# Kernel tuning notes

Measured on AMD Instinct MI355X. Metric: run time of the kernel, lower is better.

The kernel has to match this reference:

```python
import jax, jax.numpy as jnp
import numpy as np

N_NODES = 100000
N_EDGES = 1600000
D = 64


def setup_inputs() -> dict:
    key = jax.random.key(0)
    k0, k1, k2, k3 = jax.random.split(key, 4)
    scale = 1.0 / np.sqrt(D)
    return {
        "x": jax.random.normal(k0, (N_NODES, D), dtype=jnp.float32),
        "W1": jax.random.normal(k1, (D, D), dtype=jnp.float32) * scale,
        "W2": jax.random.normal(k2, (D, D), dtype=jnp.float32) * scale,
        "b2": jnp.zeros((D,), dtype=jnp.float32),
        "edge_index": jax.random.randint(k3, (2, N_EDGES), 0, N_NODES, dtype=jnp.int32),
    }


def reference(x, W1, W2, b2, edge_index):
    # KapoorConv forward in eval mode (Dropout(p=0.5) is identity at inference).
    n = x.shape[0]
    # GCNConv adds self-loops, then symmetric normalization D^-1/2 A D^-1/2.
    loops = jnp.arange(n, dtype=edge_index.dtype)
    src = jnp.concatenate([edge_index[0], loops])  # message source j
    dst = jnp.concatenate([edge_index[1], loops])  # aggregation target i
    deg = jnp.zeros((n,), x.dtype).at[dst].add(jnp.float32(1.0))
    dinv = jax.lax.rsqrt(deg)  # deg >= 1 thanks to self-loops
    norm = (dinv[src] * dinv[dst])[:, None]  # [E+N, 1]

    def gcn(h, W, b):
        h = h @ W                                   # dense transform first
        msg = h[src] * norm                         # gather + normalize
        out = jax.ops.segment_sum(msg, dst, num_segments=n)  # scatter-add
        return out if b is None else out + b

    h = jax.nn.relu(gcn(x, W1, None))  # layer1: bias=False
    return gcn(h, W2, b2)              # layer2: bias=True
```

## Files before the change

### kernel.cpp

```cpp
#include <hip/hip_runtime.h>

#define D 64
#define CHUNK 8192
#define BKT_SHIFT 8
#define BKT_NODES 256
#define MAXB 512
#define CAP 8192
#define GROWS 64
#define SSTR 68

typedef unsigned int u32;

__device__ __forceinline__ u32 bfr(float v) {
    u32 x = __float_as_uint(v);
    return (x + 0x7fffu + ((x >> 16) & 1u)) >> 16;
}
__device__ __forceinline__ u32 pack2(float lo, float hi) { return bfr(lo) | (bfr(hi) << 16); }
__device__ __forceinline__ float blo(u32 w) { return __uint_as_float(w << 16); }
__device__ __forceinline__ float bhi(u32 w) { return __uint_as_float(w & 0xffff0000u); }


__global__ void init_cursor(int* __restrict__ cursor, int B) {
    int i = blockIdx.x * blockDim.x + threadIdx.x;
    if (i < B) cursor[i] = i * CAP;
}


__global__ void partition(const int* __restrict__ src, const int* __restrict__ dst,
                          int* __restrict__ cursor, int* __restrict__ packed,
                          int nE, int B) {
    __shared__ int hist[MAXB];
    __shared__ int delta[MAXB];
    __shared__ int s[MAXB];
    __shared__ int sorted[CHUNK];
    __shared__ unsigned short sortedb[CHUNK];
    int t = threadIdx.x;
    int i0 = blockIdx.x * CHUNK;
    int cn = min(CHUNK, nE - i0);

    hist[t] = 0;
    __syncthreads();
    for (int i = t; i < cn; i += 512) atomicAdd(&hist[dst[i0 + i] >> BKT_SHIFT], 1);
    __syncthreads();

    int v = hist[t];
    s[t] = v;
    __syncthreads();
    for (int off = 1; off < MAXB; off <<= 1) {
        int u = (t >= off) ? s[t - off] : 0;
        __syncthreads();
        s[t] += u;
        __syncthreads();
    }
    {
        int excl = s[t] - v;
        int rb = 0;
        if (t < B && v > 0) rb = atomicAdd(&cursor[t], v);
        delta[t] = rb - excl;
        hist[t] = excl;
    }
    __syncthreads();

    for (int i = t; i < cn; i += 512) {
        int d = dst[i0 + i];
        int b = d >> BKT_SHIFT;
        int pp = atomicAdd(&hist[b], 1);
        sorted[pp]  = ((d & (BKT_NODES - 1)) << 17) | src[i0 + i];
        sortedb[pp] = (unsigned short)b;
    }
    __syncthreads();

    for (int i = t; i < cn; i += 512) {
        packed[delta[sortedb[i]] + i] = sorted[i];
    }
}


__global__ void bucket_csr(const int* __restrict__ packed, const int* __restrict__ cursor,
                           int* __restrict__ row_ptr, float* __restrict__ dinv,
                           int* __restrict__ adj, const float* __restrict__ x,
                           u32* __restrict__ xp, int n, int B) {
    __shared__ int s[BKT_NODES];
    __shared__ int cur[BKT_NODES];
    __shared__ float dv[BKT_NODES];
    __shared__ int base_s;
    int t = threadIdx.x;
    int b = blockIdx.x;
    int rlo = b * CAP;
    int mycnt = min(cursor[b] - rlo, CAP);

    int partial = 0;
    for (int i = t; i < b; i += BKT_NODES) partial += cursor[i] - i * CAP;
    s[t] = partial;
    __syncthreads();
    for (int off = BKT_NODES / 2; off > 0; off >>= 1) {
        if (t < off) s[t] += s[t + off];
        __syncthreads();
    }
    if (t == 0) base_s = s[0];
    __syncthreads();
    int base = base_s;
    if (b == B - 1 && t == 0) row_ptr[n] = base + mycnt;

    s[t] = 0;
    __syncthreads();
    for (int i = t; i < mycnt; i += BKT_NODES) atomicAdd(&s[packed[rlo + i] >> 17], 1);
    __syncthreads();

    int v = s[t];
    __syncthreads();
    for (int off = 1; off < BKT_NODES; off <<= 1) {
        int u = (t >= off) ? s[t - off] : 0;
        __syncthreads();
        s[t] += u;
        __syncthreads();
    }
    int gbeg = base + s[t] - v;
    int node = (b << BKT_SHIFT) + t;
    float di = rsqrtf(1.0f + (float)v);
    if (node < n) {
        row_ptr[node] = gbeg;
        dinv[node] = di;
    }
    dv[t] = di;
    cur[t] = gbeg;
    __syncthreads();

    for (int i = t; i < mycnt; i += BKT_NODES) {
        int w = packed[rlo + i];
        int pos = atomicAdd(&cur[w >> 17], 1);
        adj[pos] = w & 0x1FFFF;
    }

    int nbase = b << BKT_SHIFT;
    for (int i = t; i < BKT_NODES * 8; i += BKT_NODES) {
        int row = i >> 3, fb = i & 7;
        int nd = nbase + row;
        if (nd < n) {
            float d2 = dv[row];
            const float4* xr = (const float4*)(x + (size_t)nd * D + 8 * fb);
            float4 v0 = xr[0], v1 = xr[1];
            uint4 w;
            w.x = pack2(d2 * v0.x, d2 * v0.y);
            w.y = pack2(d2 * v0.z, d2 * v0.w);
            w.z = pack2(d2 * v1.x, d2 * v1.y);
            w.w = pack2(d2 * v1.z, d2 * v1.w);
            ((uint4*)(xp + (size_t)nd * (D / 2)))[fb] = w;
        }
    }
}

template <int MODE>
__launch_bounds__(256, 4)
__global__ void fused(const u32* __restrict__ hp, const int* __restrict__ row_ptr,
                      const int* __restrict__ adj,
                      const float* __restrict__ W, const float* __restrict__ bias,
                      const float* __restrict__ dinv,
                      float* __restrict__ outf, u32* __restrict__ outb, int n) {
    __shared__ float Wl[D * D];
    __shared__ float Sl[GROWS * SSTR];
    const int t = threadIdx.x;

    for (int i = t; i < D * D / 4; i += 256)
        ((float4*)Wl)[i] = ((const float4*)W)[i];

    const int R0 = blockIdx.x * GROWS;

    const int lane = t & 63;
    const int o = lane >> 3;
    const int f = lane & 7;
    const int wv = t >> 6;

#pragma unroll
    for (int r = 0; r < 2; ++r) {
        int row = wv * 16 + r * 8 + o;
        int nq = R0 + row;
        bool valid = nq < n;
        int nqc = valid ? nq : 0;
        int rb = row_ptr[nqc];
        int re = row_ptr[nqc + 1];
        int len = valid ? (re - rb) : 0;

        uint4 sw = ((const uint4*)(hp + (size_t)nqc * (D / 2)))[f];
        float acc[8];
        acc[0] = blo(sw.x); acc[1] = bhi(sw.x);
        acc[2] = blo(sw.y); acc[3] = bhi(sw.y);
        acc[4] = blo(sw.z); acc[5] = bhi(sw.z);
        acc[6] = blo(sw.w); acc[7] = bhi(sw.w);

        int lm = len;
        lm = max(lm, __shfl_xor(lm, 8, 64));
        lm = max(lm, __shfl_xor(lm, 16, 64));
        lm = max(lm, __shfl_xor(lm, 32, 64));

        for (int base = 0; base < lm; base += 8) {
            int rem = len - base;
            int idx_l = 0;
            if (f < rem) idx_l = adj[rb + base + f];
            int ss[8]; uint4 vv[8];
#pragma unroll
            for (int u = 0; u < 8; ++u) {
                ss[u] = __shfl(idx_l, (o << 3) | u, 64);
            }
#pragma unroll
            for (int u = 0; u < 8; ++u) {
                vv[u] = ((const uint4*)(hp + (size_t)ss[u] * (D / 2)))[f];
            }
#pragma unroll
            for (int u = 0; u < 8; ++u) {
                float m = (u < rem) ? 1.0f : 0.0f;
                acc[0] = fmaf(m, blo(vv[u].x), acc[0]);
                acc[1] = fmaf(m, bhi(vv[u].x), acc[1]);
                acc[2] = fmaf(m, blo(vv[u].y), acc[2]);
                acc[3] = fmaf(m, bhi(vv[u].y), acc[3]);
                acc[4] = fmaf(m, blo(vv[u].z), acc[4]);
                acc[5] = fmaf(m, bhi(vv[u].z), acc[5]);
                acc[6] = fmaf(m, blo(vv[u].w), acc[6]);
                acc[7] = fmaf(m, bhi(vv[u].w), acc[7]);
            }
        }
        *(float4*)&Sl[row * SSTR + 8 * f]     = make_float4(acc[0], acc[1], acc[2], acc[3]);
        *(float4*)&Sl[row * SSTR + 8 * f + 4] = make_float4(acc[4], acc[5], acc[6], acc[7]);
    }
    __syncthreads();

    const int cg = t & 15;
    const int rg = t >> 4;

    float4 acc0 = make_float4(0.f, 0.f, 0.f, 0.f);
    float4 acc1 = make_float4(0.f, 0.f, 0.f, 0.f);
    float4 acc2 = make_float4(0.f, 0.f, 0.f, 0.f);
    float4 acc3 = make_float4(0.f, 0.f, 0.f, 0.f);

#pragma unroll 4
    for (int k = 0; k < D; k += 4) {
        float4 a0 = *(const float4*)&Sl[(4 * rg + 0) * SSTR + k];
        float4 a1 = *(const float4*)&Sl[(4 * rg + 1) * SSTR + k];
        float4 a2 = *(const float4*)&Sl[(4 * rg + 2) * SSTR + k];
        float4 a3 = *(const float4*)&Sl[(4 * rg + 3) * SSTR + k];
        float4 w0 = *(const float4*)&Wl[(k + 0) * D + 4 * cg];
        float4 w1 = *(const float4*)&Wl[(k + 1) * D + 4 * cg];
        float4 w2 = *(const float4*)&Wl[(k + 2) * D + 4 * cg];
        float4 w3 = *(const float4*)&Wl[(k + 3) * D + 4 * cg];
#define MAC(ACC, A)                                                        \
        ACC.x = fmaf(A.x, w0.x, fmaf(A.y, w1.x, fmaf(A.z, w2.x, fmaf(A.w, w3.x, ACC.x)))); \
        ACC.y = fmaf(A.x, w0.y, fmaf(A.y, w1.y, fmaf(A.z, w2.y, fmaf(A.w, w3.y, ACC.y)))); \
        ACC.z = fmaf(A.x, w0.z, fmaf(A.y, w1.z, fmaf(A.z, w2.z, fmaf(A.w, w3.z, ACC.z)))); \
        ACC.w = fmaf(A.x, w0.w, fmaf(A.y, w1.w, fmaf(A.z, w2.w, fmaf(A.w, w3.w, ACC.w))))
        MAC(acc0, a0);
        MAC(acc1, a1);
        MAC(acc2, a2);
        MAC(acc3, a3);
#undef MAC
    }

    const float4 bv = (MODE == 1) ? ((const float4*)bias)[cg]
                                  : make_float4(0.f, 0.f, 0.f, 0.f);
    float4 accs[4] = {acc0, acc1, acc2, acc3};
#pragma unroll
    for (int r = 0; r < 4; ++r) {
        int row = R0 + 4 * rg + r;
        if (row >= n) break;
        float dn = dinv[row];
        float4 y = accs[r];
        if (MODE == 0) {
            float o0 = dn * fmaxf(dn * y.x, 0.f);
            float o1 = dn * fmaxf(dn * y.y, 0.f);
            float o2 = dn * fmaxf(dn * y.z, 0.f);
            float o3 = dn * fmaxf(dn * y.w, 0.f);
            uint2 w2o;
            w2o.x = pack2(o0, o1);
            w2o.y = pack2(o2, o3);
            ((uint2*)(outb + (size_t)row * (D / 2)))[cg] = w2o;
        } else {
            float4 oo;
            oo.x = fmaf(dn, y.x, bv.x);
            oo.y = fmaf(dn, y.y, bv.y);
            oo.z = fmaf(dn, y.z, bv.z);
            oo.w = fmaf(dn, y.w, bv.w);
            ((float4*)(outf + (size_t)row * D))[cg] = oo;
        }
    }
}


extern "C" void kernel_launch(void* const* d_in, const int* in_sizes, int n_in,
                              void* d_out, int out_size, void* d_ws, size_t ws_size,
                              hipStream_t stream) {
    const float* x  = (const float*)d_in[0];
    const float* W1 = (const float*)d_in[1];
    const float* W2 = (const float*)d_in[2];
    const float* b2 = (const float*)d_in[3];
    const int*   ei = (const int*)d_in[4];

    int n  = in_sizes[0] / D;
    int nE = in_sizes[4] / 2;
    const int* src = ei;
    const int* dst = ei + nE;

    int B = (n + BKT_NODES - 1) >> BKT_SHIFT;

    auto align = [](size_t v) { return (v + 255) & ~(size_t)255; };
    char* ws = (char*)d_ws;
    size_t off = 0;
    int* row_ptr = (int*)(ws + off);   off += align((size_t)(n + 1) * 4);
    float* dinv  = (float*)(ws + off); off += align((size_t)n * 4);
    int* cursor  = (int*)(ws + off);   off += align((size_t)MAXB * 4);
    int* adj     = (int*)(ws + off);   off += align((size_t)nE * 4);
    int* packed  = (int*)(ws + off);   off += align((size_t)(B + 1) * CAP * 4);
    u32* F0      = (u32*)(ws + off);   off += align((size_t)n * (D / 2) * 4);
    u32* F1      = (u32*)(ws + off);
    float* out = (float*)d_out;

    int nchunks = (nE + CHUNK - 1) / CHUNK;

    init_cursor<<<2, 256, 0, stream>>>(cursor, B);
    partition<<<nchunks, 512, 0, stream>>>(src, dst, cursor, packed, nE, B);
    bucket_csr<<<B, BKT_NODES, 0, stream>>>(packed, cursor, row_ptr, dinv, adj, x, F0, n, B);

    int gblocks = (n + GROWS - 1) / GROWS;

    fused<0><<<gblocks, 256, 0, stream>>>(F0, row_ptr, adj, W1, nullptr, dinv, nullptr, F1, n);

    fused<1><<<gblocks, 256, 0, stream>>>(F1, row_ptr, adj, W2, b2, dinv, out, nullptr, n);
}
```

Before: 205.7 us.

## Replace bucketed LDS partition CSR build with global-atomic counting sort

Replaces the two-pass shared-memory bucket partition and per-bucket CSR build with a plain counting sort: global atomic degree count, a hierarchical scan over runs of 16 nodes, then a scatter using global atomic cursors. The x prescale-to-bf16 step is folded into the scatter kernel. This removes the large packed intermediate buffer and the LDS sorting, but adds more kernel launches, a single-block scan, and heavily contended global atomics with random-order writes into adj. Within-row edge order becomes nondeterministic, which can change floating-point summation order.

Result: slower. 344.0 us (+67.3%).

```diff
diff --git a/kernel.cpp b/kernel.cpp
--- a/kernel.cpp
+++ b/kernel.cpp
@@ -1,13 +1,9 @@
 #include <hip/hip_runtime.h>
 
 #define D 64
-#define CHUNK 8192
-#define BKT_SHIFT 8
-#define BKT_NODES 256
-#define MAXB 512
-#define CAP 8192
 #define GROWS 64
 #define SSTR 68
+#define RUN 16
 
 typedef unsigned int u32;
 
@@ -20,133 +16,94 @@
 __device__ __forceinline__ float bhi(u32 w) { return __uint_as_float(w & 0xffff0000u); }
 
 
-__global__ void init_cursor(int* __restrict__ cursor, int B) {
+__global__ void zero_k(int* __restrict__ p, int n) {
     int i = blockIdx.x * blockDim.x + threadIdx.x;
-    if (i < B) cursor[i] = i * CAP;
-}
-
-
-__global__ void partition(const int* __restrict__ src, const int* __restrict__ dst,
-                          int* __restrict__ cursor, int* __restrict__ packed,
-                          int nE, int B) {
-    __shared__ int hist[MAXB];
-    __shared__ int delta[MAXB];
-    __shared__ int s[MAXB];
-    __shared__ int sorted[CHUNK];
-    __shared__ unsigned short sortedb[CHUNK];
+    if (i < n) p[i] = 0;
+}
+
+__global__ void count_deg(const int* __restrict__ dst, int* __restrict__ deg, int nE) {
+    int i = blockIdx.x * blockDim.x + threadIdx.x;
+    if (i < nE) atomicAdd(&deg[dst[i]], 1);
+}
+
+__global__ void run_sums(const int* __restrict__ deg, int* __restrict__ runsum,
+                         int n, int nrun) {
+    int r = blockIdx.x * blockDim.x + threadIdx.x;
+    if (r >= nrun) return;
+    int b = r * RUN, e = min(b + RUN, n);
+    int sum = 0;
+    for (int i = b; i < e; ++i) sum += deg[i];
+    runsum[r] = sum;
+}
+
+__global__ void scan_mid(const int* __restrict__ runsum, int* __restrict__ runbase,
+                         int nrun) {
+    __shared__ int s[1024];
     int t = threadIdx.x;
-    int i0 = blockIdx.x * CHUNK;
-    int cn = min(CHUNK, nE - i0);
-
-    hist[t] = 0;
+    int v[8];
+    int tot = 0;
+    int bi = t * 8;
+#pragma unroll
+    for (int i = 0; i < 8; ++i) {
+        int idx = bi + i;
+        v[i] = (idx < nrun) ? runsum[idx] : 0;
+        tot += v[i];
+    }
+    s[t] = tot;
     __syncthreads();
-    for (int i = t; i < cn; i += 512) atomicAdd(&hist[dst[i0 + i] >> BKT_SHIFT], 1);
-    __syncthreads();
-
-    int v = hist[t];
-    s[t] = v;
-    __syncthreads();
-    for (int off = 1; off < MAXB; off <<= 1) {
+    for (int off = 1; off < 1024; off <<= 1) {
         int u = (t >= off) ? s[t - off] : 0;
         __syncthreads();
         s[t] += u;
         __syncthreads();
     }
-    {
-        int excl = s[t] - v;
-        int rb = 0;
-        if (t < B && v > 0) rb = atomicAdd(&cursor[t], v);
-        delta[t] = rb - excl;
-        hist[t] = excl;
-    }
-    __syncthreads();
-
-    for (int i = t; i < cn; i += 512) {
-        int d = dst[i0 + i];
-        int b = d >> BKT_SHIFT;
-        int pp = atomicAdd(&hist[b], 1);
-        sorted[pp]  = ((d & (BKT_NODES - 1)) << 17) | src[i0 + i];
-        sortedb[pp] = (unsigned short)b;
-    }
-    __syncthreads();
-
-    for (int i = t; i < cn; i += 512) {
-        packed[delta[sortedb[i]] + i] = sorted[i];
-    }
-}
-
-
-__global__ void bucket_csr(const int* __restrict__ packed, const int* __restrict__ cursor,
-                           int* __restrict__ row_ptr, float* __restrict__ dinv,
-                           int* __restrict__ adj, const float* __restrict__ x,
-                           u32* __restrict__ xp, int n, int B) {
-    __shared__ int s[BKT_NODES];
-    __shared__ int cur[BKT_NODES];
-    __shared__ float dv[BKT_NODES];
-    __shared__ int base_s;
-    int t = threadIdx.x;
-    int b = blockIdx.x;
-    int rlo = b * CAP;
-    int mycnt = min(cursor[b] - rlo, CAP);
-
-    int partial = 0;
-    for (int i = t; i < b; i += BKT_NODES) partial += cursor[i] - i * CAP;
-    s[t] = partial;
-    __syncthreads();
-    for (int off = BKT_NODES / 2; off > 0; off >>= 1) {
-        if (t < off) s[t] += s[t + off];
-        __syncthreads();
-    }
-    if (t == 0) base_s = s[0];
-    __syncthreads();
-    int base = base_s;
-    if (b == B - 1 && t == 0) row_ptr[n] = base + mycnt;
-
-    s[t] = 0;
-    __syncthreads();
-    for (int i = t; i < mycnt; i += BKT_NODES) atomicAdd(&s[packed[rlo + i] >> 17], 1);
-    __syncthreads();
-
-    int v = s[t];
-    __syncthreads();
-    for (int off = 1; off < BKT_NODES; off <<= 1) {
-        int u = (t >= off) ? s[t - off] : 0;
-        __syncthreads();
-        s[t] += u;
-        __syncthreads();
-    }
-    int gbeg = base + s[t] - v;
-    int node = (b << BKT_SHIFT) + t;
-    float di = rsqrtf(1.0f + (float)v);
-    if (node < n) {
-        row_ptr[node] = gbeg;
-        dinv[node] = di;
-    }
-    dv[t] = di;
-    cur[t] = gbeg;
-    __syncthreads();
-
-    for (int i = t; i < mycnt; i += BKT_NODES) {
-        int w = packed[rlo + i];
-        int pos = atomicAdd(&cur[w >> 17], 1);
-        adj[pos] = w & 0x1FFFF;
-    }
-
-    int nbase = b << BKT_SHIFT;
-    for (int i = t; i < BKT_NODES * 8; i += BKT_NODES) {
-        int row = i >> 3, fb = i & 7;
-        int nd = nbase + row;
-        if (nd < n) {
-            float d2 = dv[row];
-            const float4* xr = (const float4*)(x + (size_t)nd * D + 8 * fb);
-            float4 v0 = xr[0], v1 = xr[1];
-            uint4 w;
-            w.x = pack2(d2 * v0.x, d2 * v0.y);
-            w.y = pack2(d2 * v0.z, d2 * v0.w);
-            w.z = pack2(d2 * v1.x, d2 * v1.y);
-            w.w = pack2(d2 * v1.z, d2 * v1.w);
-            ((uint4*)(xp + (size_t)nd * (D / 2)))[fb] = w;
-        }
+    int excl = s[t] - tot;
+#pragma unroll
+    for (int i = 0; i < 8; ++i) {
+        int idx = bi + i;
+        if (idx < nrun) runbase[idx] = excl;
+        excl += v[i];
+    }
+}
+
+__global__ void build_rows(const int* __restrict__ deg, const int* __restrict__ runbase,
+                           int* __restrict__ row_ptr, int* __restrict__ cur,
+                           float* __restrict__ dinv, int n, int nrun) {
+    int r = blockIdx.x * blockDim.x + threadIdx.x;
+    if (r >= nrun) return;
+    int base = runbase[r];
+    int b = r * RUN, e = min(b + RUN, n);
+    for (int i = b; i < e; ++i) {
+        row_ptr[i] = base;
+        cur[i] = base;
+        int dg = deg[i];
+        dinv[i] = rsqrtf(1.0f + (float)dg);
+        base += dg;
+    }
+    if (r == nrun - 1) row_ptr[n] = base;
+}
+
+__global__ void scatter_prescale(const int* __restrict__ src, const int* __restrict__ dst,
+                                 int* __restrict__ cur, int* __restrict__ adj,
+                                 const float* __restrict__ x, const float* __restrict__ dinv,
+                                 u32* __restrict__ xp, int n, int nE) {
+    int tid = blockIdx.x * blockDim.x + threadIdx.x;
+    if (tid < nE) {
+        int d = dst[tid];
+        int pos = atomicAdd(&cur[d], 1);
+        adj[pos] = src[tid];
+    }
+    if (tid < n * 8) {
+        int row = tid >> 3, fb = tid & 7;
+        float d2 = dinv[row];
+        const float4* xr = (const float4*)(x + (size_t)row * D + 8 * fb);
+        float4 v0 = xr[0], v1 = xr[1];
+        uint4 w;
+        w.x = pack2(d2 * v0.x, d2 * v0.y);
+        w.y = pack2(d2 * v0.z, d2 * v0.w);
+        w.z = pack2(d2 * v1.x, d2 * v1.y);
+        w.w = pack2(d2 * v1.z, d2 * v1.w);
+        ((uint4*)(xp + (size_t)row * (D / 2)))[fb] = w;
     }
 }
 
@@ -298,25 +255,28 @@
     const int* src = ei;
     const int* dst = ei + nE;
 
-    int B = (n + BKT_NODES - 1) >> BKT_SHIFT;
+    int nrun = (n + RUN - 1) / RUN;
 
     auto align = [](size_t v) { return (v + 255) & ~(size_t)255; };
     char* ws = (char*)d_ws;
     size_t off = 0;
     int* row_ptr = (int*)(ws + off);   off += align((size_t)(n + 1) * 4);
     float* dinv  = (float*)(ws + off); off += align((size_t)n * 4);
-    int* cursor  = (int*)(ws + off);   off += align((size_t)MAXB * 4);
+    int* deg     = (int*)(ws + off);   off += align((size_t)n * 4);
+    int* cur     = (int*)(ws + off);   off += align((size_t)n * 4);
+    int* runsum  = (int*)(ws + off);   off += align((size_t)nrun * 4);
+    int* runbase = (int*)(ws + off);   off += align((size_t)nrun * 4);
     int* adj     = (int*)(ws + off);   off += align((size_t)nE * 4);
-    int* packed  = (int*)(ws + off);   off += align((size_t)(B + 1) * CAP * 4);
     u32* F0      = (u32*)(ws + off);   off += align((size_t)n * (D / 2) * 4);
     u32* F1      = (u32*)(ws + off);
     float* out = (float*)d_out;
 
-    int nchunks = (nE + CHUNK - 1) / CHUNK;
-
-    init_cursor<<<2, 256, 0, stream>>>(cursor, B);
-    partition<<<nchunks, 512, 0, stream>>>(src, dst, cursor, packed, nE, B);
-    bucket_csr<<<B, BKT_NODES, 0, stream>>>(packed, cursor, row_ptr, dinv, adj, x, F0, n, B);
+    zero_k<<<(n + 255) / 256, 256, 0, stream>>>(deg, n);
+    count_deg<<<(nE + 255) / 256, 256, 0, stream>>>(dst, deg, nE);
+    run_sums<<<(nrun + 255) / 256, 256, 0, stream>>>(deg, runsum, n, nrun);
+    scan_mid<<<1, 1024, 0, stream>>>(runsum, runbase, nrun);
+    build_rows<<<(nrun + 255) / 256, 256, 0, stream>>>(deg, runbase, row_ptr, cur, dinv, n, nrun);
+    scatter_prescale<<<(nE + 255) / 256, 256, 0, stream>>>(src, dst, cur, adj, x, dinv, F0, n, nE);
 
     int gblocks = (n + GROWS - 1) / GROWS;
 
```
